# Kernel tuning notes

Measured on AMD Instinct MI355X. Metric: run time of the kernel, lower is better.

The kernel has to match this reference:

```python
import jax, jax.numpy as jnp
import numpy as np

D_MODEL = 1024
N_HEADS = 16
HEAD_DIM = D_MODEL // N_HEADS


def setup_inputs() -> dict:
    key = jax.random.key(0)
    ks = jax.random.split(key, 5)
    T, B = 2048, 2
    scale = 1.0 / np.sqrt(D_MODEL)
    x = jax.random.normal(ks[0], (T, B, D_MODEL), dtype=jnp.float32)
    W_qkv = jax.random.normal(ks[1], (D_MODEL, 3 * D_MODEL), dtype=jnp.float32) * scale
    b_qkv = jnp.zeros((3 * D_MODEL,), dtype=jnp.float32)
    W_out = jax.random.normal(ks[2], (D_MODEL, D_MODEL), dtype=jnp.float32) * scale
    b_out = jnp.zeros((D_MODEL,), dtype=jnp.float32)
    return {"x": x, "W_qkv": W_qkv, "b_qkv": b_qkv, "W_out": W_out, "b_out": b_out}


def reference(x, W_qkv, b_qkv, W_out, b_out):
    T, B, D = x.shape
    H, Dh = N_HEADS, HEAD_DIM
    qkv = x @ W_qkv + b_qkv  # [T, B, 3D]
    q, k, v = jnp.split(qkv, 3, axis=-1)
    # [T, B, D] -> [B, H, T, Dh]
    def to_heads(t):
        return t.reshape(T, B, H, Dh).transpose(1, 2, 0, 3)
    q, k, v = to_heads(q), to_heads(k), to_heads(v)
    scores = jnp.einsum("bhqd,bhkd->bhqk", q, k) / jnp.sqrt(jnp.float32(Dh))
    causal = jnp.tril(jnp.ones((T, T), dtype=bool))  # True where attention allowed
    scores = jnp.where(causal, scores, -jnp.inf)
    attn = jax.nn.softmax(scores, axis=-1)
    context = jnp.einsum("bhqk,bhkd->bhqd", attn, v)  # [B, H, T, Dh]
    context = context.transpose(2, 0, 1, 3).reshape(T, B, D)  # [T, B, D]
    return context @ W_out + b_out
```

## Files before the change

### kernel.cpp

```cpp
#include <hip/hip_runtime.h>
#include <stdint.h>

#define T_SEQ 2048
#define BATCH 2
#define DMODEL 1024
#define NH 16
#define DH 64
#define M_ROWS (T_SEQ * BATCH)
#define N_QKV (3 * DMODEL)

typedef unsigned short u16;
using bf16x8 = __attribute__((ext_vector_type(8))) __bf16;
using f32x4  = __attribute__((ext_vector_type(4))) float;

__device__ __forceinline__ u16 f2bf(float f) {
    union { float f; uint32_t u; } v; v.f = f;
    uint32_t r = v.u + 0x7fffu + ((v.u >> 16) & 1u);
    return (u16)(r >> 16);
}

__device__ __forceinline__ uint32_t pack2(float a, float b) {
    union { float f; uint32_t u; } x, y; x.f = a; y.f = b;
    return (x.u >> 16) | (y.u & 0xffff0000u);
}

__device__ __forceinline__ float bf2f(u16 u) {
    union { uint32_t u; float f; } v; v.u = (uint32_t)u << 16;
    return v.f;
}

__device__ __forceinline__ void lds_load16(void* lds, const void* g) {
    auto lp = (__attribute__((address_space(3))) uint32_t*)(uint32_t)(uintptr_t)lds;
    auto gp = (const __attribute__((address_space(1))) uint32_t*)(uintptr_t)g;
    __builtin_amdgcn_global_load_lds(gp, lp, 16, 0, 0);
}

#define SCQ 0.18033688011112f


__global__ void prep_kernel(const float* __restrict__ x, u16* __restrict__ xb,
                            const float* __restrict__ Wq, u16* __restrict__ oq,
                            const float* __restrict__ Wo, u16* __restrict__ oo) {
    __shared__ float t[32][33];
    if (blockIdx.x < 4096) {
        int i = blockIdx.x * 256 + threadIdx.x;
        float4 v = ((const float4*)x)[i];
        union { u16 u[4]; uint2 d; } o;
        o.u[0] = f2bf(v.x); o.u[1] = f2bf(v.y); o.u[2] = f2bf(v.z); o.u[3] = f2bf(v.w);
        ((uint2*)xb)[i] = o.d;
    } else {
        const int R = 1024;
        int bxx = blockIdx.x - 4096;
        int gx = bxx & 127, gy = bxx >> 7;
        const float* in; u16* out; int C, bx;
        if (gx < 96) { in = Wq; out = oq; C = 3072; bx = gx * 32; }
        else         { in = Wo; out = oo; C = 1024; bx = (gx - 96) * 32; }
        int by = gy * 32;
        int tx = threadIdx.x & 31, ty = threadIdx.x >> 5;
#pragma unroll
        for (int rr = 0; rr < 32; rr += 8)
            t[ty + rr][tx] = in[(size_t)(by + ty + rr) * C + bx + tx];
        __syncthreads();
#pragma unroll
        for (int rr = 0; rr < 32; rr += 8)
            out[(size_t)(bx + ty + rr) * R + by + tx] = f2bf(t[tx][ty + rr]);
    }
}


template<int EPI, int NF>
__global__ __launch_bounds__(256) void gemm_kernel(
    const u16* __restrict__ A, const u16* __restrict__ Bt,
    const float* __restrict__ bias,
    u16* __restrict__ outQ, u16* __restrict__ outK, u16* __restrict__ outV,
    float* __restrict__ outF,
    int M, int N, int K)
{
    __shared__ __align__(16) u16 lA[2][128 * 32];
    __shared__ __align__(16) u16 lB[2][NF * 32 * 32];

    const int tid  = threadIdx.x;
    const int bm   = blockIdx.y * 128;
    const int bn   = blockIdx.x * (NF * 32);
    const int lane = tid & 63;
    const int wid  = tid >> 6;
    const int wm   = (wid >> 1) * 64;
    const int wn   = (wid & 1) * (NF * 16);
    const int qr   = lane & 15;
    const int quad = lane >> 4;
    const int r4   = lane >> 2;
    const int c4   = (((lane & 3) ^ ((r4 >> 1) & 3))) * 8;
    const int sw   = (qr >> 1) & 3;

    f32x4 acc[4][NF];
#pragma unroll
    for (int i = 0; i < 4; i++)
#pragma unroll
        for (int j = 0; j < NF; j++) acc[i][j] = f32x4{0.f, 0.f, 0.f, 0.f};

#pragma unroll
    for (int cc = 0; cc < 2; cc++) {
        int c = wid + cc * 4;
        lds_load16(&lA[0][c * 512], &A[(size_t)(bm + 16 * c + r4) * K + c4]);
    }
#pragma unroll
    for (int c = wid; c < 2 * NF; c += 4)
        lds_load16(&lB[0][c * 512], &Bt[(size_t)(bn + 16 * c + r4) * K + c4]);

    int p = 0;
    for (int k0 = 0; k0 < K; k0 += 32, p ^= 1) {
        __syncthreads();
        if (k0 + 32 < K) {
            int nb = p ^ 1;
#pragma unroll
            for (int cc = 0; cc < 2; cc++) {
                int c = wid + cc * 4;
                lds_load16(&lA[nb][c * 512], &A[(size_t)(bm + 16 * c + r4) * K + k0 + 32 + c4]);
            }
#pragma unroll
            for (int c = wid; c < 2 * NF; c += 4)
                lds_load16(&lB[nb][c * 512], &Bt[(size_t)(bn + 16 * c + r4) * K + k0 + 32 + c4]);
        }

        bf16x8 af[4], bfr[NF];
#pragma unroll
        for (int i = 0; i < 4; i++)
            af[i] = *(const bf16x8*)&lA[p][(wm + i * 16 + qr) * 32 + ((quad ^ sw) * 8)];
#pragma unroll
        for (int j = 0; j < NF; j++)
            bfr[j] = *(const bf16x8*)&lB[p][(wn + j * 16 + qr) * 32 + ((quad ^ sw) * 8)];
#pragma unroll
        for (int i = 0; i < 4; i++)
#pragma unroll
            for (int j = 0; j < NF; j++)
                acc[i][j] = __builtin_amdgcn_mfma_f32_16x16x32_bf16(af[i], bfr[j], acc[i][j], 0, 0, 0);
    }

#pragma unroll
    for (int i = 0; i < 4; i++) {
#pragma unroll
        for (int j = 0; j < NF; j++) {
            int col = bn + wn + j * 16 + qr;
            float bv = bias[col];
#pragma unroll
            for (int r = 0; r < 4; r++) {
                int row = bm + wm + i * 16 + quad * 4 + r;
                float val = acc[i][j][r] + bv;
                if (EPI == 0) {
                    int t = row >> 1, b = row & 1;
                    int which = col >> 10;
                    int dm = col & 1023;
                    int h = dm >> 6, dh = dm & 63;
                    int bh = b * NH + h;
                    if (which == 0) {
                        outQ[((size_t)bh * T_SEQ + t) * DH + dh] = f2bf(val * SCQ);
                    } else if (which == 1) {
                        outK[((size_t)bh * T_SEQ + t) * DH + dh] = f2bf(val);
                    } else {
                        outV[((size_t)bh * DH + dh) * T_SEQ + t] = f2bf(val);
                    }
                } else {
                    outF[(size_t)row * N + col] = val;
                }
            }
        }
    }
}


__global__ __launch_bounds__(256) void attn_kernel(
    const u16* __restrict__ Qb, const u16* __restrict__ Kb,
    const u16* __restrict__ Vt, u16* __restrict__ ctx)
{
    __shared__ __align__(16) u16 lK[2][64 * 64];
    __shared__ __align__(16) u16 lV[2][64 * 64];
    __shared__ __align__(16) u16 lP[4][16 * 64];

    const int bh   = blockIdx.x;
    const int y    = blockIdx.y;
    const int qt   = (y < 16) ? 31 - y : y - 16;
    const int tid  = threadIdx.x;
    const int lane = tid & 63;
    const int wid  = tid >> 6;
    const int qr   = lane & 15;
    const int quad = lane >> 4;
    const int sw   = qr & 7;

    const int srow = wid * 8 + (lane >> 3);
    const int scol = (((lane & 7) ^ ((lane >> 3) & 7))) * 8;

    const u16* Q  = Qb + (size_t)bh * T_SEQ * DH;
    const u16* Kp = Kb + (size_t)bh * T_SEQ * DH;
    const u16* Vp = Vt + (size_t)bh * DH * T_SEQ;
    const int b = bh >> 4, h = bh & 15;

    const int q0 = qt * 64 + wid * 16;

    bf16x8 qf[2];
#pragma unroll
    for (int ks = 0; ks < 2; ks++)
        qf[ks] = *(const bf16x8*)&Q[(size_t)(q0 + qr) * DH + ks * 32 + quad * 8];

    bf16x8 onesf;
#pragma unroll
    for (int j = 0; j < 8; j++) onesf[j] = (__bf16)1.0f;

    f32x4 o[5];
#pragma unroll
    for (int f = 0; f < 5; f++) o[f] = f32x4{0.f, 0.f, 0.f, 0.f};

    const int NT = qt + 1;

    lds_load16(&lK[0][wid * 512],        &Kp[(size_t)srow * DH + scol]);
    lds_load16(&lK[0][2048 + wid * 512], &Kp[(size_t)(32 + srow) * DH + scol]);
    lds_load16(&lV[0][wid * 512],        &Vp[(size_t)srow * T_SEQ + scol]);
    lds_load16(&lV[0][2048 + wid * 512], &Vp[(size_t)(32 + srow) * T_SEQ + scol]);

    int p = 0;
    for (int kt = 0; kt < NT; kt++, p ^= 1) {
        __syncthreads();
        if (kt + 1 < NT) {
            int nb = p ^ 1;
            lds_load16(&lK[nb][wid * 512],        &Kp[(size_t)((kt + 1) * 64 + srow) * DH + scol]);
            lds_load16(&lK[nb][2048 + wid * 512], &Kp[(size_t)((kt + 1) * 64 + 32 + srow) * DH + scol]);
            lds_load16(&lV[nb][wid * 512],        &Vp[(size_t)srow * T_SEQ + (kt + 1) * 64 + scol]);
            lds_load16(&lV[nb][2048 + wid * 512], &Vp[(size_t)(32 + srow) * T_SEQ + (kt + 1) * 64 + scol]);
        }
        if (kt * 64 > q0 + 15) continue;

        f32x4 s[4];
#pragma unroll
        for (int fn = 0; fn < 4; fn++) s[fn] = f32x4{0.f, 0.f, 0.f, 0.f};
        __builtin_amdgcn_s_setprio(1);
#pragma unroll
        for (int fn = 0; fn < 4; fn++)
#pragma unroll
            for (int ks = 0; ks < 2; ks++) {
                bf16x8 kf = *(const bf16x8*)&lK[p][(fn * 16 + qr) * 64 + (((ks * 4 + quad) ^ sw) * 8)];
                s[fn] = __builtin_amdgcn_mfma_f32_16x16x32_bf16(kf, qf[ks], s[fn], 0, 0, 0);
            }
        __builtin_amdgcn_s_setprio(0);

        if (kt * 64 + 63 > q0) {
            int q = q0 + qr;
#pragma unroll
            for (int fn = 0; fn < 4; fn++) {
                int key = kt * 64 + fn * 16 + quad * 4;
#pragma unroll
                for (int r = 0; r < 4; r++)
                    if (key + r > q) s[fn][r] = -1e30f;
            }
        }

        bf16x8 pf[2];
#pragma unroll
        for (int fn = 0; fn < 4; fn++) {
            float p0 = exp2f(s[fn][0]);
            float p1 = exp2f(s[fn][1]);
            float p2 = exp2f(s[fn][2]);
            float p3 = exp2f(s[fn][3]);
            uint2 w; w.x = pack2(p0, p1); w.y = pack2(p2, p3);
            int phys = ((fn * 2 + (quad >> 1)) ^ sw);
            *(uint2*)&lP[wid][qr * 64 + phys * 8 + (quad & 1) * 4] = w;
        }
#pragma unroll
        for (int ks = 0; ks < 2; ks++)
            pf[ks] = *(const bf16x8*)&lP[wid][qr * 64 + (((ks * 4 + quad) ^ sw) * 8)];

        __builtin_amdgcn_s_setprio(1);
#pragma unroll
        for (int f = 0; f < 5; f++)
#pragma unroll
            for (int ks = 0; ks < 2; ks++) {
                bf16x8 vf = (f == 4) ? onesf
                    : *(const bf16x8*)&lV[p][(f * 16 + qr) * 64 + (((ks * 4 + quad) ^ sw) * 8)];
                o[f] = __builtin_amdgcn_mfma_f32_16x16x32_bf16(vf, pf[ks], o[f], 0, 0, 0);
            }
        __builtin_amdgcn_s_setprio(0);
    }

    {
        int q = q0 + qr;
        float invl = 1.0f / o[4][0];
#pragma unroll
        for (int f = 0; f < 4; f++) {
            uint2 w;
            w.x = (uint32_t)f2bf(o[f][0] * invl) | ((uint32_t)f2bf(o[f][1] * invl) << 16);
            w.y = (uint32_t)f2bf(o[f][2] * invl) | ((uint32_t)f2bf(o[f][3] * invl) << 16);
            *(uint2*)&ctx[((size_t)q * BATCH + b) * DMODEL + h * DH + f * 16 + quad * 4] = w;
        }
    }
}


extern "C" void kernel_launch(void* const* d_in, const int* in_sizes, int n_in,
                              void* d_out, int out_size, void* d_ws, size_t ws_size,
                              hipStream_t stream) {
    const float* x     = (const float*)d_in[0];
    const float* W_qkv = (const float*)d_in[1];
    const float* b_qkv = (const float*)d_in[2];
    const float* W_out = (const float*)d_in[3];
    const float* b_out = (const float*)d_in[4];
    float* out = (float*)d_out;

    char* ws = (char*)d_ws;
    u16* xb     = (u16*)(ws + 0);
    u16* wqkv_t = (u16*)(ws + (8u  << 20));
    u16* wout_t = (u16*)(ws + (14u << 20));
    u16* Qb     = (u16*)(ws + (16u << 20));
    u16* Kb     = (u16*)(ws + (24u << 20));
    u16* Vt     = (u16*)(ws + (32u << 20));
    u16* ctx    = xb;

    prep_kernel<<<8192, 256, 0, stream>>>(x, xb, W_qkv, wqkv_t, W_out, wout_t);

    gemm_kernel<0, 4><<<dim3(N_QKV / 128, M_ROWS / 128), 256, 0, stream>>>(
        xb, wqkv_t, b_qkv, Qb, Kb, Vt, nullptr, M_ROWS, N_QKV, DMODEL);

    attn_kernel<<<dim3(BATCH * NH, T_SEQ / 64), 256, 0, stream>>>(
        Qb, Kb, Vt, ctx);

    gemm_kernel<1, 2><<<dim3(DMODEL / 64, M_ROWS / 128), 256, 0, stream>>>(
        ctx, wout_t, b_out, nullptr, nullptr, nullptr, out, M_ROWS, DMODEL, DMODEL);
}
```

Before: 177.3 us.

## Add ping-pong pipelined QKV GEMM with 128x192 tiles and K=64 stages

Replaces the templated QKV projection GEMM with a dedicated kernel that uses 128x192 output tiles, a K step of 64, and XOR-swizzled LDS layout. Global-to-LDS prefetches of the next tile are interleaved between phases of MFMA work with explicit barriers and waitcnt, so loads overlap compute. Larger tiles raise data reuse per LDS load but use more LDS (about 80KB) and more accumulators, which can limit occupancy. The grid shrinks to 16x32 blocks.

```diff
diff --git a/kernel.cpp b/kernel.cpp
--- a/kernel.cpp
+++ b/kernel.cpp
@@ -36,6 +36,10 @@
 }
 
 #define SCQ 0.18033688011112f
+
+#define SBAR()       asm volatile("s_barrier" ::: "memory")
+#define WAIT_LGKM0() asm volatile("s_waitcnt lgkmcnt(0)" ::: "memory")
+#define WAIT_VM0()   asm volatile("s_waitcnt vmcnt(0)" ::: "memory")
 
 
 __global__ void prep_kernel(const float* __restrict__ x, u16* __restrict__ xb,
@@ -68,6 +72,137 @@
 }
 
 
+__global__ __launch_bounds__(256) void gemm8p_kernel(
+    const u16* __restrict__ A, const u16* __restrict__ Bt,
+    const float* __restrict__ bias,
+    u16* __restrict__ outQ, u16* __restrict__ outK, u16* __restrict__ outV)
+{
+    __shared__ __align__(16) u16 lA[2][128 * 64];
+    __shared__ __align__(16) u16 lB[2][192 * 64];
+
+    const int tid  = threadIdx.x;
+    const int lane = tid & 63;
+    const int wid  = tid >> 6;
+    const int wm   = (wid >> 1) * 64;
+    const int wn   = (wid & 1) * 96;
+    const int qr   = lane & 15;
+    const int quad = lane >> 4;
+    const int sw   = qr & 7;
+
+    const int bm = blockIdx.y * 128;
+    const int bn = blockIdx.x * 192;
+    const int K  = DMODEL;
+
+    const int srow = tid >> 3;
+    const int lch  = (tid & 7) ^ (srow & 7);
+
+    f32x4 acc[4][6];
+#pragma unroll
+    for (int i = 0; i < 4; i++)
+#pragma unroll
+        for (int j = 0; j < 6; j++) acc[i][j] = f32x4{0.f, 0.f, 0.f, 0.f};
+
+    const int NTILES = K / 64;
+
+#define STAGE_A(BUF, C, U) lds_load16(&lA[BUF][(C) * 2048 + wid * 512], \
+        &A[(size_t)(bm + (C) * 32 + srow) * K + (U) * 64 + lch * 8])
+#define STAGE_B(BUF, C, U) lds_load16(&lB[BUF][(C) * 2048 + wid * 512], \
+        &Bt[(size_t)(bn + (C) * 32 + srow) * K + (U) * 64 + lch * 8])
+
+#pragma unroll
+    for (int c = 0; c < 4; c++) STAGE_A(0, c, 0);
+#pragma unroll
+    for (int c = 0; c < 6; c++) STAGE_B(0, c, 0);
+    WAIT_VM0();
+    SBAR();
+
+    bf16x8 af[4], bq[3];
+
+#define READ_A(KS)                                                              \
+    _Pragma("unroll")                                                           \
+    for (int i = 0; i < 4; i++)                                                 \
+        af[i] = *(const bf16x8*)&lA[p][(wm + i * 16 + qr) * 64 +                \
+                                       ((((KS) * 4 + quad) ^ sw) * 8)];
+#define READ_B(J0, KS)                                                          \
+    _Pragma("unroll")                                                           \
+    for (int j = 0; j < 3; j++)                                                 \
+        bq[j] = *(const bf16x8*)&lB[p][(wn + ((J0) + j) * 16 + qr) * 64 +       \
+                                       ((((KS) * 4 + quad) ^ sw) * 8)];
+#define MFMA12(J0)                                                              \
+    _Pragma("unroll")                                                           \
+    for (int i = 0; i < 4; i++)                                                 \
+        _Pragma("unroll")                                                       \
+        for (int j = 0; j < 3; j++)                                             \
+            acc[i][(J0) + j] = __builtin_amdgcn_mfma_f32_16x16x32_bf16(         \
+                af[i], bq[j], acc[i][(J0) + j], 0, 0, 0);
+
+    int p = 0;
+#pragma unroll 1
+    for (int u = 0; u < NTILES; u++, p ^= 1) {
+        const int np = p ^ 1;
+        const bool pf = (u + 1 < NTILES);
+
+        READ_A(0) READ_B(0, 0)
+        if (pf) { STAGE_B(np, 0, u + 1); STAGE_B(np, 1, u + 1);
+                  STAGE_B(np, 2, u + 1); STAGE_B(np, 3, u + 1); }
+        SBAR(); WAIT_LGKM0();
+        MFMA12(0)
+        SBAR();
+
+        READ_B(3, 0)
+        if (pf) { STAGE_B(np, 4, u + 1); STAGE_B(np, 5, u + 1);
+                  STAGE_A(np, 0, u + 1); }
+        SBAR(); WAIT_LGKM0();
+        MFMA12(3)
+        SBAR();
+
+        READ_A(1) READ_B(0, 1)
+        if (pf) { STAGE_A(np, 1, u + 1); STAGE_A(np, 2, u + 1);
+                  STAGE_A(np, 3, u + 1); }
+        SBAR(); WAIT_LGKM0();
+        MFMA12(0)
+        SBAR();
+
+        READ_B(3, 1)
+        SBAR(); WAIT_LGKM0();
+        MFMA12(3)
+        if (pf) WAIT_VM0();
+        SBAR();
+    }
+#undef READ_A
+#undef READ_B
+#undef MFMA12
+#undef STAGE_A
+#undef STAGE_B
+
+#pragma unroll
+    for (int i = 0; i < 4; i++) {
+#pragma unroll
+        for (int j = 0; j < 6; j++) {
+            int col = bn + wn + j * 16 + qr;
+            float bv = bias[col];
+            int which = col >> 10;
+            int dm = col & 1023;
+            int h = dm >> 6, dh = dm & 63;
+#pragma unroll
+            for (int r = 0; r < 4; r++) {
+                int row = bm + wm + i * 16 + quad * 4 + r;
+                float val = acc[i][j][r] + bv;
+                int t = row >> 1, b = row & 1;
+                int bh = b * NH + h;
+                if (which == 0) {
+                    outQ[((size_t)bh * T_SEQ + t) * DH + dh] = f2bf(val * SCQ);
+                } else if (which == 1) {
+                    outK[((size_t)bh * T_SEQ + t) * DH + dh] = f2bf(val);
+                } else {
+                    outV[((size_t)bh * DH + dh) * T_SEQ + t] = f2bf(val);
+                }
+            }
+        }
+    }
+}
+
+
 template<int EPI, int NF>
 __global__ __launch_bounds__(256) void gemm_kernel(
     const u16* __restrict__ A, const u16* __restrict__ Bt,
@@ -314,8 +449,8 @@
 
     prep_kernel<<<8192, 256, 0, stream>>>(x, xb, W_qkv, wqkv_t, W_out, wout_t);
 
-    gemm_kernel<0, 4><<<dim3(N_QKV / 128, M_ROWS / 128), 256, 0, stream>>>(
-        xb, wqkv_t, b_qkv, Qb, Kb, Vt, nullptr, M_ROWS, N_QKV, DMODEL);
+    gemm8p_kernel<<<dim3(N_QKV / 192, M_ROWS / 128), 256, 0, stream>>>(
+        xb, wqkv_t, b_qkv, Qb, Kb, Vt);
 
     attn_kernel<<<dim3(BATCH * NH, T_SEQ / 64), 256, 0, stream>>>(
         Qb, Kb, Vt, ctx);
```

Result: slower. 197.1 us (+11.1%).

## Process two 16-row query groups per wave to reuse K/V tiles

Applied to the files above, without the earlier changes.

Each attention block now covers 128 query rows instead of 64, and each wave handles two 16-row query groups that share every K and V fragment read from LDS. This halves the grid and the number of times each K/V tile is staged per query, cutting LDS and global traffic per unit of MFMA work. The cost is twice the accumulator and score registers per wave and fewer blocks in flight, which may reduce occupancy. The causal-skip check now works at 32-row granularity, so some fully masked work is done.

```diff
diff --git a/kernel.cpp b/kernel.cpp
--- a/kernel.cpp
+++ b/kernel.cpp
@@ -178,7 +178,7 @@
 
     const int bh   = blockIdx.x;
     const int y    = blockIdx.y;
-    const int qt   = (y < 16) ? 31 - y : y - 16;
+    const int qt   = (y < 8) ? 15 - y : y - 8;
     const int tid  = threadIdx.x;
     const int lane = tid & 63;
     const int wid  = tid >> 6;
@@ -194,22 +194,26 @@
     const u16* Vp = Vt + (size_t)bh * DH * T_SEQ;
     const int b = bh >> 4, h = bh & 15;
 
-    const int q0 = qt * 64 + wid * 16;
-
-    bf16x8 qf[2];
-#pragma unroll
-    for (int ks = 0; ks < 2; ks++)
-        qf[ks] = *(const bf16x8*)&Q[(size_t)(q0 + qr) * DH + ks * 32 + quad * 8];
+    const int q0 = qt * 128 + wid * 32;
+
+    bf16x8 qf[2][2];
+#pragma unroll
+    for (int g = 0; g < 2; g++)
+#pragma unroll
+        for (int ks = 0; ks < 2; ks++)
+            qf[g][ks] = *(const bf16x8*)&Q[(size_t)(q0 + g * 16 + qr) * DH + ks * 32 + quad * 8];
 
     bf16x8 onesf;
 #pragma unroll
     for (int j = 0; j < 8; j++) onesf[j] = (__bf16)1.0f;
 
-    f32x4 o[5];
-#pragma unroll
-    for (int f = 0; f < 5; f++) o[f] = f32x4{0.f, 0.f, 0.f, 0.f};
-
-    const int NT = qt + 1;
+    f32x4 o[2][5];
+#pragma unroll
+    for (int g = 0; g < 2; g++)
+#pragma unroll
+        for (int f = 0; f < 5; f++) o[g][f] = f32x4{0.f, 0.f, 0.f, 0.f};
+
+    const int NT = 2 * (qt + 1);
 
     lds_load16(&lK[0][wid * 512],        &Kp[(size_t)srow * DH + scol]);
     lds_load16(&lK[0][2048 + wid * 512], &Kp[(size_t)(32 + srow) * DH + scol]);
@@ -226,46 +230,56 @@
             lds_load16(&lV[nb][wid * 512],        &Vp[(size_t)srow * T_SEQ + (kt + 1) * 64 + scol]);
             lds_load16(&lV[nb][2048 + wid * 512], &Vp[(size_t)(32 + srow) * T_SEQ + (kt + 1) * 64 + scol]);
         }
-        if (kt * 64 > q0 + 15) continue;
-
-        f32x4 s[4];
-#pragma unroll
-        for (int fn = 0; fn < 4; fn++) s[fn] = f32x4{0.f, 0.f, 0.f, 0.f};
+        if (kt * 64 > q0 + 31) continue;
+
+        f32x4 s[2][4];
+#pragma unroll
+        for (int g = 0; g < 2; g++)
+#pragma unroll
+            for (int fn = 0; fn < 4; fn++) s[g][fn] = f32x4{0.f, 0.f, 0.f, 0.f};
         __builtin_amdgcn_s_setprio(1);
 #pragma unroll
         for (int fn = 0; fn < 4; fn++)
 #pragma unroll
             for (int ks = 0; ks < 2; ks++) {
                 bf16x8 kf = *(const bf16x8*)&lK[p][(fn * 16 + qr) * 64 + (((ks * 4 + quad) ^ sw) * 8)];
-                s[fn] = __builtin_amdgcn_mfma_f32_16x16x32_bf16(kf, qf[ks], s[fn], 0, 0, 0);
+#pragma unroll
+                for (int g = 0; g < 2; g++)
+                    s[g][fn] = __builtin_amdgcn_mfma_f32_16x16x32_bf16(kf, qf[g][ks], s[g][fn], 0, 0, 0);
             }
         __builtin_amdgcn_s_setprio(0);
 
         if (kt * 64 + 63 > q0) {
-            int q = q0 + qr;
+#pragma unroll
+            for (int g = 0; g < 2; g++) {
+                int q = q0 + g * 16 + qr;
+#pragma unroll
+                for (int fn = 0; fn < 4; fn++) {
+                    int key = kt * 64 + fn * 16 + quad * 4;
+#pragma unroll
+                    for (int r = 0; r < 4; r++)
+                        if (key + r > q) s[g][fn][r] = -1e30f;
+                }
+            }
+        }
+
+        bf16x8 pf[2][2];
+#pragma unroll
+        for (int g = 0; g < 2; g++) {
 #pragma unroll
             for (int fn = 0; fn < 4; fn++) {
-                int key = kt * 64 + fn * 16 + quad * 4;
-#pragma unroll
-                for (int r = 0; r < 4; r++)
-                    if (key + r > q) s[fn][r] = -1e30f;
-            }
-        }
-
-        bf16x8 pf[2];
-#pragma unroll
-        for (int fn = 0; fn < 4; fn++) {
-            float p0 = exp2f(s[fn][0]);
-            float p1 = exp2f(s[fn][1]);
-            float p2 = exp2f(s[fn][2]);
-            float p3 = exp2f(s[fn][3]);
-            uint2 w; w.x = pack2(p0, p1); w.y = pack2(p2, p3);
-            int phys = ((fn * 2 + (quad >> 1)) ^ sw);
-            *(uint2*)&lP[wid][qr * 64 + phys * 8 + (quad & 1) * 4] = w;
-        }
-#pragma unroll
-        for (int ks = 0; ks < 2; ks++)
-            pf[ks] = *(const bf16x8*)&lP[wid][qr * 64 + (((ks * 4 + quad) ^ sw) * 8)];
+                float p0 = exp2f(s[g][fn][0]);
+                float p1 = exp2f(s[g][fn][1]);
+                float p2 = exp2f(s[g][fn][2]);
+                float p3 = exp2f(s[g][fn][3]);
+                uint2 w; w.x = pack2(p0, p1); w.y = pack2(p2, p3);
+                int phys = ((fn * 2 + (quad >> 1)) ^ sw);
+                *(uint2*)&lP[wid][qr * 64 + phys * 8 + (quad & 1) * 4] = w;
+            }
+#pragma unroll
+            for (int ks = 0; ks < 2; ks++)
+                pf[g][ks] = *(const bf16x8*)&lP[wid][qr * 64 + (((ks * 4 + quad) ^ sw) * 8)];
+        }
 
         __builtin_amdgcn_s_setprio(1);
 #pragma unroll
@@ -274,19 +288,22 @@
             for (int ks = 0; ks < 2; ks++) {
                 bf16x8 vf = (f == 4) ? onesf
                     : *(const bf16x8*)&lV[p][(f * 16 + qr) * 64 + (((ks * 4 + quad) ^ sw) * 8)];
-                o[f] = __builtin_amdgcn_mfma_f32_16x16x32_bf16(vf, pf[ks], o[f], 0, 0, 0);
+#pragma unroll
+                for (int g = 0; g < 2; g++)
+                    o[g][f] = __builtin_amdgcn_mfma_f32_16x16x32_bf16(vf, pf[g][ks], o[g][f], 0, 0, 0);
             }
         __builtin_amdgcn_s_setprio(0);
     }
 
-    {
-        int q = q0 + qr;
-        float invl = 1.0f / o[4][0];
+#pragma unroll
+    for (int g = 0; g < 2; g++) {
+        int q = q0 + g * 16 + qr;
+        float invl = 1.0f / o[g][4][0];
 #pragma unroll
         for (int f = 0; f < 4; f++) {
             uint2 w;
-            w.x = (uint32_t)f2bf(o[f][0] * invl) | ((uint32_t)f2bf(o[f][1] * invl) << 16);
-            w.y = (uint32_t)f2bf(o[f][2] * invl) | ((uint32_t)f2bf(o[f][3] * invl) << 16);
+            w.x = (uint32_t)f2bf(o[g][f][0] * invl) | ((uint32_t)f2bf(o[g][f][1] * invl) << 16);
+            w.y = (uint32_t)f2bf(o[g][f][2] * invl) | ((uint32_t)f2bf(o[g][f][3] * invl) << 16);
             *(uint2*)&ctx[((size_t)q * BATCH + b) * DMODEL + h * DH + f * 16 + quad * 4] = w;
         }
     }
@@ -317,7 +334,7 @@
     gemm_kernel<0, 4><<<dim3(N_QKV / 128, M_ROWS / 128), 256, 0, stream>>>(
         xb, wqkv_t, b_qkv, Qb, Kb, Vt, nullptr, M_ROWS, N_QKV, DMODEL);
 
-    attn_kernel<<<dim3(BATCH * NH, T_SEQ / 64), 256, 0, stream>>>(
+    attn_kernel<<<dim3(BATCH * NH, T_SEQ / 128), 256, 0, stream>>>(
         Qb, Kb, Vt, ctx);
 
     gemm_kernel<1, 2><<<dim3(DMODEL / 64, M_ROWS / 128), 256, 0, stream>>>(
```

After: 191.0 us. +7.7%, slower.
